# Kernel optimization log

Measured on AMD Instinct MI355X. Metric: run time of the kernel, lower is better.

The kernel has to match this reference:

```python
import jax, jax.numpy as jnp
import numpy as np

N = 20000      # total nodes (miRNA_number); first 504 are circRNAs
FM = 128       # feature dim (args.fm)
H = 8          # attention heads
OC = 128       # conv out_channels
E = 160000     # random edges (self loops added inside reference)
NEG_SLOPE = 0.2
CIRC = 504


def setup_inputs() -> dict:
    key = jax.random.key(0)
    ks = jax.random.split(key, 12)
    s_in = 1.0 / np.sqrt(FM)
    return {
        'x': jax.random.normal(ks[0], (N, FM), jnp.float32),
        'edge_index': jax.random.randint(ks[1], (2, E), 0, N, jnp.int64),
        'W1': jax.random.normal(ks[2], (FM, H * FM), jnp.float32) * s_in,
        'as1': jax.random.normal(ks[3], (H, FM), jnp.float32) * 0.1,
        'ad1': jax.random.normal(ks[4], (H, FM), jnp.float32) * 0.1,
        'b1': jnp.zeros((FM,), jnp.float32),
        'W2': jax.random.normal(ks[5], (FM, H * FM), jnp.float32) * s_in,
        'as2': jax.random.normal(ks[6], (H, FM), jnp.float32) * 0.1,
        'ad2': jax.random.normal(ks[7], (H, FM), jnp.float32) * 0.1,
        'b2': jnp.zeros((FM,), jnp.float32),
        'Wc': jax.random.normal(ks[8], (OC, 2, FM), jnp.float32) * s_in,
        'bc': jnp.zeros((OC,), jnp.float32),
    }


def gat_conv(x, src, dst, W, a_src, a_dst, b):
    # PyG GATConv, heads=H, concat=False (head mean), add_self_loops done by caller
    h = (x @ W).reshape(N, H, FM)                       # [N,H,F]
    s = jnp.einsum('nhf,hf->nh', h, a_src)              # alpha_src per node
    d = jnp.einsum('nhf,hf->nh', h, a_dst)              # alpha_dst per node
    e = jax.nn.leaky_relu(s[src] + d[dst], NEG_SLOPE)   # [E,H]
    m = jax.ops.segment_max(e, dst, num_segments=N)     # segment softmax (stable)
    ee = jnp.exp(e - m[dst])
    den = jax.ops.segment_sum(ee, dst, num_segments=N)
    alpha = ee / (den[dst] + 1e-16)                     # [E,H]
    out = jax.ops.segment_sum(h[src] * alpha[:, :, None], dst, num_segments=N)
    return out.mean(axis=1) + b                         # [N,F]


def reference(x, edge_index, W1, as1, ad1, b1, W2, as2, ad2, b2, Wc, bc):
    loops = jnp.arange(N, dtype=edge_index.dtype)
    src = jnp.concatenate([edge_index[0], loops])
    dst = jnp.concatenate([edge_index[1], loops])
    x1 = jax.nn.relu(gat_conv(x, src, dst, W1, as1, ad1, b1))
    x2 = jax.nn.relu(gat_conv(x1, src, dst, W2, as2, ad2, b2))
    # cat((x1,x2),dim=1).t().view(1, 2, FM, N) -> channels = [x1.T, x2.T]
    XM = jnp.stack([x1.T, x2.T], axis=0)                # [2,FM,N]
    feat = jnp.einsum('ckn,ock->on', XM, Wc) + bc[:, None]  # Conv1d kernel (FM,1)
    emb = feat.T                                        # [N,OC]
    circ, mir = emb[:CIRC], emb[CIRC:]
    return circ @ mir.T, circ, mir
```

## Files before the change

kernel.cpp:

```cpp
#include <hip/hip_runtime.h>
#include <math.h>

constexpr int NN   = 20000;
constexpr int FM   = 128;
constexpr int NH   = 8;
constexpr int HF   = NH * FM;
constexpr int EE   = 160000;
constexpr int ET   = EE + NN;
constexpr int OC   = 128;
constexpr int CIRC = 504;
constexpr int MIRN = NN - CIRC;
constexpr float NEG = 0.2f;

constexpr size_t OFF_CIRC = (size_t)CIRC * MIRN;
constexpr size_t OFF_MIR  = OFF_CIRC + (size_t)CIRC * OC;

typedef __attribute__((ext_vector_type(8))) short bf16x8;
typedef __attribute__((ext_vector_type(4))) float f32x4;

__device__ __forceinline__ int rl_i(int v, int lane) {
  return __builtin_amdgcn_readlane(v, lane);
}
__device__ __forceinline__ unsigned short bf16_rne(float x) {
  unsigned u = __float_as_uint(x);
  return (unsigned short)((u + 0x7FFFu + ((u >> 16) & 1u)) >> 16);
}
__device__ __forceinline__ float blo(unsigned u) { return __uint_as_float(u << 16); }
__device__ __forceinline__ float bhi(unsigned u) { return __uint_as_float(u & 0xFFFF0000u); }

__global__ void k_init_counts(int* __restrict__ cnt) {
  int i = blockIdx.x * blockDim.x + threadIdx.x;
  if (i < NN) cnt[i] = 1;
}

__global__ void k_count(const int* __restrict__ ei, int* __restrict__ cnt) {
  int e = blockIdx.x * blockDim.x + threadIdx.x;
  if (e < EE) atomicAdd(&cnt[ei[EE + e]], 1);
}

__global__ __launch_bounds__(1024) void k_scan(const int* __restrict__ cnt,
                                               int* __restrict__ rs,
                                               int* __restrict__ cur) {
  __shared__ int part[1024];
  const int t = threadIdx.x;
  const int SEG = (NN + 1023) / 1024;
  int lo = t * SEG, hi = min(NN, lo + SEG);
  int s = 0;
  for (int i = lo; i < hi; ++i) s += cnt[i];
  part[t] = s;
  __syncthreads();
  for (int off = 1; off < 1024; off <<= 1) {
    int v = 0;
    if (t >= off) v = part[t - off];
    __syncthreads();
    part[t] += v;
    __syncthreads();
  }
  int run = (t == 0) ? 0 : part[t - 1];
  for (int i = lo; i < hi; ++i) {
    int c = cnt[i];
    rs[i] = run;
    cur[i] = run;
    run += c;
  }
  if (t == 1023) rs[NN] = part[1023];
}

__global__ void k_fill(const int* __restrict__ ei, int* __restrict__ cur,
                       int* __restrict__ csrc) {
  int i = blockIdx.x * blockDim.x + threadIdx.x;
  if (i >= ET) return;
  int s, d;
  if (i < EE) { s = ei[i]; d = ei[EE + i]; }
  else        { s = i - EE; d = s; }
  int p = atomicAdd(&cur[d], 1);
  csrc[p] = s;
}

__global__ void k_prep_w(const float* __restrict__ W,
                         unsigned short* __restrict__ WThi,
                         unsigned short* __restrict__ WTlo) {
  int i = blockIdx.x * blockDim.x + threadIdx.x;
  if (i >= FM * HF) return;
  int k = i >> 10, n = i & 1023;
  float v = W[i];
  unsigned short h = bf16_rne(v);
  WThi[(size_t)n * FM + k] = h;
  WTlo[(size_t)n * FM + k] = bf16_rne(v - blo(h));
}

__global__ void k_split_x(const float* __restrict__ X,
                          unsigned short* __restrict__ Xhi,
                          unsigned short* __restrict__ Xlo) {
  int i = blockIdx.x * blockDim.x + threadIdx.x;
  if (i >= NN * FM) return;
  float v = X[i];
  unsigned short h = bf16_rne(v);
  Xhi[i] = h;
  Xlo[i] = bf16_rne(v - blo(h));
}

__global__ __launch_bounds__(256) void k_gemm_mfma(
    const unsigned short* __restrict__ Xhi, const unsigned short* __restrict__ Xlo,
    const unsigned short* __restrict__ WThi, const unsigned short* __restrict__ WTlo,
    const float* __restrict__ Asc, const float* __restrict__ Adc,
    unsigned short* __restrict__ H16, float* __restrict__ Sv,
    float* __restrict__ Dv) {
  const int lane = threadIdx.x & 63;
  const int wq   = threadIdx.x >> 6;
  const int m0   = blockIdx.x * 16;
  const int ri   = lane & 15;
  const int kg   = lane >> 4;

  bf16x8 Ah[4], Al[4];
  const unsigned short* xb = Xhi + (size_t)(m0 + ri) * FM + kg * 8;
  const unsigned short* xl = Xlo + (size_t)(m0 + ri) * FM + kg * 8;
#pragma unroll
  for (int ks = 0; ks < 4; ++ks) {
    Ah[ks] = *reinterpret_cast<const bf16x8*>(xb + ks * 32);
    Al[ks] = *reinterpret_cast<const bf16x8*>(xl + ks * 32);
  }
  float sacc[2][4] = {}, dacc[2][4] = {};
  for (int ct = 0; ct < 16; ++ct) {
    const int gc = wq * 256 + ct * 16 + ri;
    const unsigned short* wb = WThi + (size_t)gc * FM + kg * 8;
    const unsigned short* wl = WTlo + (size_t)gc * FM + kg * 8;
    f32x4 a0 = {0.f, 0.f, 0.f, 0.f}, a1 = a0, a2 = a0;
#pragma unroll
    for (int ks = 0; ks < 4; ++ks) {
      bf16x8 Bh = *reinterpret_cast<const bf16x8*>(wb + ks * 32);
      bf16x8 Bl = *reinterpret_cast<const bf16x8*>(wl + ks * 32);
      a0 = __builtin_amdgcn_mfma_f32_16x16x32_bf16(Ah[ks], Bh, a0, 0, 0, 0);
      a1 = __builtin_amdgcn_mfma_f32_16x16x32_bf16(Al[ks], Bh, a1, 0, 0, 0);
      a2 = __builtin_amdgcn_mfma_f32_16x16x32_bf16(Ah[ks], Bl, a2, 0, 0, 0);
    }
    const int hh = ct >> 3;
    const float as_ = Asc[(wq * 2 + hh) * FM + (gc & 127)];
    const float ad_ = Adc[(wq * 2 + hh) * FM + (gc & 127)];
#pragma unroll
    for (int r = 0; r < 4; ++r) {
      float v = a0[r] + a1[r] + a2[r];
      int m = m0 + kg * 4 + r;
      H16[(size_t)m * HF + gc] = bf16_rne(v);
      sacc[hh][r] += v * as_;
      dacc[hh][r] += v * ad_;
    }
  }
#pragma unroll
  for (int hh = 0; hh < 2; ++hh)
#pragma unroll
    for (int r = 0; r < 4; ++r) {
      float s = sacc[hh][r], d = dacc[hh][r];
#pragma unroll
      for (int mo = 1; mo <= 8; mo <<= 1) {
        s += __shfl_xor(s, mo, 64);
        d += __shfl_xor(d, mo, 64);
      }
      if (ri == 0) {
        int m = m0 + kg * 4 + r;
        Sv[m * NH + wq * 2 + hh] = s;
        Dv[m * NH + wq * 2 + hh] = d;
      }
    }
}

__global__ __launch_bounds__(256) void k_agg(const unsigned short* __restrict__ H16,
                                             const float* __restrict__ Sv,
                                             const float* __restrict__ Dv,
                                             const int* __restrict__ rs,
                                             const int* __restrict__ csrc,
                                             const float* __restrict__ bias,
                                             float* __restrict__ Xo,
                                             unsigned short* __restrict__ XhiO,
                                             unsigned short* __restrict__ XloO) {
  const int wave = threadIdx.x >> 6;
  const int lane = threadIdx.x & 63;
  const int n = blockIdx.x * 4 + wave;
  if (n >= NN) return;
  const int r0 = rs[n];
  const int deg = rs[n + 1] - r0;
  const int j = lane >> 3, h = lane & 7;
  const int h0 = lane >> 4;
  const int boff = h0 * FM + (lane & 15) * 8;
  const float dvh = Dv[n * 8 + h];

  float m = -INFINITY, l = 0.f;
  float4 acc[4];
#pragma unroll
  for (int q = 0; q < 4; ++q) acc[q] = make_float4(0.f, 0.f, 0.f, 0.f);

  for (int base = 0; base < deg; base += 8) {
    const int cnt = deg - base;
    int sj = csrc[r0 + min(base + j, deg - 1)];
    float lg = (j < cnt) ? (Sv[sj * 8 + h] + dvh) : -INFINITY;
    lg = lg > 0.f ? lg : NEG * lg;
    float cm = lg;
    cm = fmaxf(cm, __shfl_xor(cm, 8, 64));
    cm = fmaxf(cm, __shfl_xor(cm, 16, 64));
    cm = fmaxf(cm, __shfl_xor(cm, 32, 64));
    float mn = fmaxf(m, cm);
    float fs = expf(m - mn);
    float p = expf(lg - mn);
    float cs = p;
    cs += __shfl_xor(cs, 8, 64);
    cs += __shfl_xor(cs, 16, 64);
    cs += __shfl_xor(cs, 32, 64);
    l = l * fs + cs;
    m = mn;
    float f0 = __shfl(fs, h0, 64);
    float f1 = __shfl(fs, h0 + 4, 64);
    acc[0].x *= f0; acc[0].y *= f0; acc[0].z *= f0; acc[0].w *= f0;
    acc[1].x *= f0; acc[1].y *= f0; acc[1].z *= f0; acc[1].w *= f0;
    acc[2].x *= f1; acc[2].y *= f1; acc[2].z *= f1; acc[2].w *= f1;
    acc[3].x *= f1; acc[3].y *= f1; acc[3].z *= f1; acc[3].w *= f1;
#pragma unroll
    for (int jj = 0; jj < 8; ++jj) {
      if (jj < cnt) {
        int se = rl_i(sj, jj * 8);
        const uint4* hp = reinterpret_cast<const uint4*>(H16 + (size_t)se * HF + boff);
        uint4 v0 = hp[0];
        uint4 v1 = hp[64];
        float pe0 = __shfl(p, jj * 8 + h0, 64);
        float pe1 = __shfl(p, jj * 8 + h0 + 4, 64);
        acc[0].x += pe0 * blo(v0.x); acc[0].y += pe0 * bhi(v0.x);
        acc[0].z += pe0 * blo(v0.y); acc[0].w += pe0 * bhi(v0.y);
        acc[1].x += pe0 * blo(v0.z); acc[1].y += pe0 * bhi(v0.z);
        acc[1].z += pe0 * blo(v0.w); acc[1].w += pe0 * bhi(v0.w);
        acc[2].x += pe1 * blo(v1.x); acc[2].y += pe1 * bhi(v1.x);
        acc[2].z += pe1 * blo(v1.y); acc[2].w += pe1 * bhi(v1.y);
        acc[3].x += pe1 * blo(v1.z); acc[3].y += pe1 * bhi(v1.z);
        acc[3].z += pe1 * blo(v1.w); acc[3].w += pe1 * bhi(v1.w);
      }
    }
  }
  float inv0 = 1.0f / (__shfl(l, h0, 64) + 1e-16f);
  float inv1 = 1.0f / (__shfl(l, h0 + 4, 64) + 1e-16f);
  float o[8];
  o[0] = acc[0].x * inv0 + acc[2].x * inv1;
  o[1] = acc[0].y * inv0 + acc[2].y * inv1;
  o[2] = acc[0].z * inv0 + acc[2].z * inv1;
  o[3] = acc[0].w * inv0 + acc[2].w * inv1;
  o[4] = acc[1].x * inv0 + acc[3].x * inv1;
  o[5] = acc[1].y * inv0 + acc[3].y * inv1;
  o[6] = acc[1].z * inv0 + acc[3].z * inv1;
  o[7] = acc[1].w * inv0 + acc[3].w * inv1;
#pragma unroll
  for (int k = 0; k < 8; ++k) {
    o[k] += __shfl_xor(o[k], 16, 64);
    o[k] += __shfl_xor(o[k], 32, 64);
  }
  if (lane < 16) {
    const int f0i = lane * 8;
    float vals[8];
    union { unsigned short us[8]; uint4 v; } ph, pl;
#pragma unroll
    for (int k = 0; k < 8; ++k) {
      float bv = bias[f0i + k];
      vals[k] = fmaxf(o[k] * 0.125f + bv, 0.f);
      unsigned short hh = bf16_rne(vals[k]);
      ph.us[k] = hh;
      pl.us[k] = bf16_rne(vals[k] - blo(hh));
    }
    float4 w0 = make_float4(vals[0], vals[1], vals[2], vals[3]);
    float4 w1 = make_float4(vals[4], vals[5], vals[6], vals[7]);
    *reinterpret_cast<float4*>(Xo + (size_t)n * FM + f0i) = w0;
    *reinterpret_cast<float4*>(Xo + (size_t)n * FM + f0i + 4) = w1;
    *reinterpret_cast<uint4*>(XhiO + (size_t)n * FM + f0i) = ph.v;
    *reinterpret_cast<uint4*>(XloO + (size_t)n * FM + f0i) = pl.v;
  }
}

__global__ void k_transpose_wc(const float* __restrict__ Wc, float* __restrict__ WcT) {
  int i = blockIdx.x * blockDim.x + threadIdx.x;
  if (i < OC * 2 * FM) {
    int o = i / (2 * FM), k = i % (2 * FM);
    WcT[k * OC + o] = Wc[i];
  }
}

__global__ __launch_bounds__(256) void k_emb(const float* __restrict__ X1,
                                             const float* __restrict__ X2,
                                             const float* __restrict__ WcT,
                                             const float* __restrict__ bc,
                                             float* __restrict__ Out) {
  __shared__ float xs[64][129];
  const int t = threadIdx.x;
  const int row0 = blockIdx.x * 64;
  const int tr = (t >> 5) << 3;
  const int tc = (t & 31) << 2;
  float acc[8][4] = {};
  for (int half = 0; half < 2; ++half) {
    const float* Xs = half ? X2 : X1;
    __syncthreads();
#pragma unroll
    for (int it = 0; it < 8; ++it) {
      int f4 = it * 256 + t;
      int r = f4 >> 5;
      int c = (f4 & 31) << 2;
      int gr = row0 + r;
      float4 v = make_float4(0.f, 0.f, 0.f, 0.f);
      if (gr < NN) v = *reinterpret_cast<const float4*>(Xs + (size_t)gr * FM + c);
      xs[r][c] = v.x; xs[r][c + 1] = v.y; xs[r][c + 2] = v.z; xs[r][c + 3] = v.w;
    }
    __syncthreads();
    const float* Wp = WcT + (size_t)half * FM * OC;
    for (int kk = 0; kk < FM; ++kk) {
      float4 b = *reinterpret_cast<const float4*>(Wp + kk * OC + tc);
      float av[8];
#pragma unroll
      for (int r = 0; r < 8; ++r) av[r] = xs[tr + r][kk];
#pragma unroll
      for (int r = 0; r < 8; ++r) {
        acc[r][0] += av[r] * b.x;
        acc[r][1] += av[r] * b.y;
        acc[r][2] += av[r] * b.z;
        acc[r][3] += av[r] * b.w;
      }
    }
  }
  float4 bcv = *reinterpret_cast<const float4*>(bc + tc);
#pragma unroll
  for (int r = 0; r < 8; ++r) {
    int gr = row0 + tr + r;
    if (gr < NN) {
      float4 o;
      o.x = acc[r][0] + bcv.x;
      o.y = acc[r][1] + bcv.y;
      o.z = acc[r][2] + bcv.z;
      o.w = acc[r][3] + bcv.w;
      float* dst = (gr < CIRC)
                       ? (Out + OFF_CIRC + (size_t)gr * OC + tc)
                       : (Out + OFF_MIR + (size_t)(gr - CIRC) * OC + tc);
      *reinterpret_cast<float4*>(dst) = o;
    }
  }
}

__global__ __launch_bounds__(256) void k_outer(const float* __restrict__ A,
                                               const float* __restrict__ B,
                                               float* __restrict__ C) {
  __shared__ float As[64][65];
  __shared__ float Bs[64][65];
  const int t = threadIdx.x;
  const int i0 = blockIdx.y * 64;
  const int j0 = blockIdx.x * 64;
  const int tx = t & 15, ty = t >> 4;
  float acc[4][4] = {};
  for (int kh = 0; kh < 2; ++kh) {
    __syncthreads();
#pragma unroll
    for (int it = 0; it < 4; ++it) {
      int f4 = it * 256 + t;
      int r = f4 >> 4;
      int c = (f4 & 15) << 2;
      float4 v = make_float4(0.f, 0.f, 0.f, 0.f);
      if (i0 + r < CIRC)
        v = *reinterpret_cast<const float4*>(A + (size_t)(i0 + r) * OC + kh * 64 + c);
      As[r][c] = v.x; As[r][c + 1] = v.y; As[r][c + 2] = v.z; As[r][c + 3] = v.w;
      float4 w = make_float4(0.f, 0.f, 0.f, 0.f);
      if (j0 + r < MIRN)
        w = *reinterpret_cast<const float4*>(B + (size_t)(j0 + r) * OC + kh * 64 + c);
      Bs[r][c] = w.x; Bs[r][c + 1] = w.y; Bs[r][c + 2] = w.z; Bs[r][c + 3] = w.w;
    }
    __syncthreads();
    for (int kk = 0; kk < 64; ++kk) {
      float a[4], b[4];
#pragma unroll
      for (int r = 0; r < 4; ++r) a[r] = As[ty * 4 + r][kk];
#pragma unroll
      for (int c = 0; c < 4; ++c) b[c] = Bs[tx * 4 + c][kk];
#pragma unroll
      for (int r = 0; r < 4; ++r)
#pragma unroll
        for (int c = 0; c < 4; ++c) acc[r][c] += a[r] * b[c];
    }
  }
#pragma unroll
  for (int r = 0; r < 4; ++r) {
    int i = i0 + ty * 4 + r;
    if (i >= CIRC) break;
#pragma unroll
    for (int c = 0; c < 4; ++c) {
      int j = j0 + tx * 4 + c;
      if (j < MIRN) C[(size_t)i * MIRN + j] = acc[r][c];
    }
  }
}

static inline size_t alignup(size_t v) { return (v + 255) & ~(size_t)255; }

extern "C" void kernel_launch(void* const* d_in, const int* in_sizes, int n_in,
                              void* d_out, int out_size, void* d_ws, size_t ws_size,
                              hipStream_t stream) {
  const float* x   = (const float*)d_in[0];
  const int*   ei  = (const int*)d_in[1];
  const float* W1  = (const float*)d_in[2];
  const float* as1 = (const float*)d_in[3];
  const float* ad1 = (const float*)d_in[4];
  const float* b1  = (const float*)d_in[5];
  const float* W2  = (const float*)d_in[6];
  const float* as2 = (const float*)d_in[7];
  const float* ad2 = (const float*)d_in[8];
  const float* b2  = (const float*)d_in[9];
  const float* Wc  = (const float*)d_in[10];
  const float* bc  = (const float*)d_in[11];
  float* out = (float*)d_out;

  char* w = (char*)d_ws;
  size_t off = 0;
  unsigned short* H16  = (unsigned short*)(w + off); off = alignup(off + (size_t)NN * HF * 2);
  unsigned short* Xhi  = (unsigned short*)(w + off); off = alignup(off + (size_t)NN * FM * 2);
  unsigned short* Xlo  = (unsigned short*)(w + off); off = alignup(off + (size_t)NN * FM * 2);
  unsigned short* WThi = (unsigned short*)(w + off); off = alignup(off + (size_t)HF * FM * 2);
  unsigned short* WTlo = (unsigned short*)(w + off); off = alignup(off + (size_t)HF * FM * 2);
  float* Sbuf = (float*)(w + off); off = alignup(off + (size_t)NN * NH * 4);
  float* Dbuf = (float*)(w + off); off = alignup(off + (size_t)NN * NH * 4);
  float* X1   = (float*)(w + off); off = alignup(off + (size_t)NN * FM * 4);
  float* X2   = (float*)(w + off); off = alignup(off + (size_t)NN * FM * 4);
  float* WcT  = (float*)(w + off); off = alignup(off + (size_t)OC * 2 * FM * 4);
  int* counts = (int*)(w + off);   off = alignup(off + (size_t)NN * 4);
  int* rowst  = (int*)(w + off);   off = alignup(off + (size_t)(NN + 1) * 4);
  int* cursor = (int*)(w + off);   off = alignup(off + (size_t)NN * 4);
  int* csrsrc = (int*)(w + off);   off = alignup(off + (size_t)ET * 4);

  k_init_counts<<<(NN + 255) / 256, 256, 0, stream>>>(counts);
  k_count<<<(EE + 255) / 256, 256, 0, stream>>>(ei, counts);
  k_scan<<<1, 1024, 0, stream>>>(counts, rowst, cursor);
  k_fill<<<(ET + 255) / 256, 256, 0, stream>>>(ei, cursor, csrsrc);

  k_prep_w<<<(FM * HF + 255) / 256, 256, 0, stream>>>(W1, WThi, WTlo);
  k_split_x<<<(NN * FM + 255) / 256, 256, 0, stream>>>(x, Xhi, Xlo);
  k_gemm_mfma<<<NN / 16, 256, 0, stream>>>(Xhi, Xlo, WThi, WTlo, as1, ad1,
                                           H16, Sbuf, Dbuf);
  k_agg<<<(NN + 3) / 4, 256, 0, stream>>>(H16, Sbuf, Dbuf, rowst, csrsrc, b1,
                                          X1, Xhi, Xlo);
  k_prep_w<<<(FM * HF + 255) / 256, 256, 0, stream>>>(W2, WThi, WTlo);
  k_gemm_mfma<<<NN / 16, 256, 0, stream>>>(Xhi, Xlo, WThi, WTlo, as2, ad2,
                                           H16, Sbuf, Dbuf);
  k_agg<<<(NN + 3) / 4, 256, 0, stream>>>(H16, Sbuf, Dbuf, rowst, csrsrc, b2,
                                          X2, Xhi, Xlo);
  k_transpose_wc<<<(OC * 2 * FM + 255) / 256, 256, 0, stream>>>(Wc, WcT);
  k_emb<<<(NN + 63) / 64, 256, 0, stream>>>(X1, X2, WcT, bc, out);
  k_outer<<<dim3((MIRN + 63) / 64, (CIRC + 63) / 64), 256, 0, stream>>>(
      out + OFF_CIRC, out + OFF_MIR, out);
}
```

Measured before the change: 560.7 us.

## Retile projection GEMM into 64x64 per-wave tiles with atomic attention-score reduction

The feature-projection GEMM moves from 16-row blocks, where each wave streamed 256 columns, to a 2D grid in which each wave computes a 64x64 output tile from register-held A and B fragments. Each loaded fragment now feeds four MFMAs instead of one. Because a head's 128 columns are split across two waves, the per-node source and destination attention scores are accumulated with atomicAdd into buffers that a new kernel zeroes before each GEMM. This adds a zeroing launch and atomic traffic, raises register pressure from 16 accumulators, and makes the float summation order of the scores nondeterministic.

```diff
diff --git a/kernel.cpp b/kernel.cpp
--- a/kernel.cpp
+++ b/kernel.cpp
@@ -100,6 +100,11 @@
   Xlo[i] = bf16_rne(v - blo(h));
 }
 
+__global__ void k_zero_sd(float* __restrict__ Sv, float* __restrict__ Dv) {
+  int i = blockIdx.x * blockDim.x + threadIdx.x;
+  if (i < NN * NH) { Sv[i] = 0.f; Dv[i] = 0.f; }
+}
+
 __global__ __launch_bounds__(256) void k_gemm_mfma(
     const unsigned short* __restrict__ Xhi, const unsigned short* __restrict__ Xlo,
     const unsigned short* __restrict__ WThi, const unsigned short* __restrict__ WTlo,
@@ -107,61 +112,83 @@
     unsigned short* __restrict__ H16, float* __restrict__ Sv,
     float* __restrict__ Dv) {
   const int lane = threadIdx.x & 63;
-  const int wq   = threadIdx.x >> 6;
-  const int m0   = blockIdx.x * 16;
+  const int w    = threadIdx.x >> 6;
+  const int m0   = blockIdx.x * 64;
+  const int c0   = blockIdx.y * 256 + w * 64;
   const int ri   = lane & 15;
   const int kg   = lane >> 4;
 
-  bf16x8 Ah[4], Al[4];
-  const unsigned short* xb = Xhi + (size_t)(m0 + ri) * FM + kg * 8;
-  const unsigned short* xl = Xlo + (size_t)(m0 + ri) * FM + kg * 8;
-#pragma unroll
+  f32x4 acc[4][4];
+#pragma unroll
+  for (int mt = 0; mt < 4; ++mt)
+#pragma unroll
+    for (int nt = 0; nt < 4; ++nt) acc[mt][nt] = {0.f, 0.f, 0.f, 0.f};
+
   for (int ks = 0; ks < 4; ++ks) {
-    Ah[ks] = *reinterpret_cast<const bf16x8*>(xb + ks * 32);
-    Al[ks] = *reinterpret_cast<const bf16x8*>(xl + ks * 32);
-  }
-  float sacc[2][4] = {}, dacc[2][4] = {};
-  for (int ct = 0; ct < 16; ++ct) {
-    const int gc = wq * 256 + ct * 16 + ri;
-    const unsigned short* wb = WThi + (size_t)gc * FM + kg * 8;
-    const unsigned short* wl = WTlo + (size_t)gc * FM + kg * 8;
-    f32x4 a0 = {0.f, 0.f, 0.f, 0.f}, a1 = a0, a2 = a0;
-#pragma unroll
-    for (int ks = 0; ks < 4; ++ks) {
-      bf16x8 Bh = *reinterpret_cast<const bf16x8*>(wb + ks * 32);
-      bf16x8 Bl = *reinterpret_cast<const bf16x8*>(wl + ks * 32);
-      a0 = __builtin_amdgcn_mfma_f32_16x16x32_bf16(Ah[ks], Bh, a0, 0, 0, 0);
-      a1 = __builtin_amdgcn_mfma_f32_16x16x32_bf16(Al[ks], Bh, a1, 0, 0, 0);
-      a2 = __builtin_amdgcn_mfma_f32_16x16x32_bf16(Ah[ks], Bl, a2, 0, 0, 0);
-    }
-    const int hh = ct >> 3;
-    const float as_ = Asc[(wq * 2 + hh) * FM + (gc & 127)];
-    const float ad_ = Adc[(wq * 2 + hh) * FM + (gc & 127)];
+    const int ko = ks * 32 + kg * 8;
+    bf16x8 Ah[4], Al[4], Bh[4], Bl[4];
+#pragma unroll
+    for (int mt = 0; mt < 4; ++mt) {
+      int row = min(m0 + mt * 16 + ri, NN - 1);
+      Ah[mt] = *reinterpret_cast<const bf16x8*>(Xhi + (size_t)row * FM + ko);
+      Al[mt] = *reinterpret_cast<const bf16x8*>(Xlo + (size_t)row * FM + ko);
+    }
+#pragma unroll
+    for (int nt = 0; nt < 4; ++nt) {
+      int col = c0 + nt * 16 + ri;
+      Bh[nt] = *reinterpret_cast<const bf16x8*>(WThi + (size_t)col * FM + ko);
+      Bl[nt] = *reinterpret_cast<const bf16x8*>(WTlo + (size_t)col * FM + ko);
+    }
+#pragma unroll
+    for (int mt = 0; mt < 4; ++mt)
+#pragma unroll
+      for (int nt = 0; nt < 4; ++nt) {
+        acc[mt][nt] = __builtin_amdgcn_mfma_f32_16x16x32_bf16(Ah[mt], Bh[nt], acc[mt][nt], 0, 0, 0);
+        acc[mt][nt] = __builtin_amdgcn_mfma_f32_16x16x32_bf16(Al[mt], Bh[nt], acc[mt][nt], 0, 0, 0);
+        acc[mt][nt] = __builtin_amdgcn_mfma_f32_16x16x32_bf16(Ah[mt], Bl[nt], acc[mt][nt], 0, 0, 0);
+      }
+  }
+
+  const int hd   = c0 >> 7;
+  const int cih0 = c0 & 127;
+  float asv[4], adv[4];
+#pragma unroll
+  for (int nt = 0; nt < 4; ++nt) {
+    int cih = cih0 + nt * 16 + ri;
+    asv[nt] = Asc[hd * FM + cih];
+    adv[nt] = Adc[hd * FM + cih];
+  }
+#pragma unroll
+  for (int mt = 0; mt < 4; ++mt) {
+    float ssum[4] = {0.f, 0.f, 0.f, 0.f};
+    float dsum[4] = {0.f, 0.f, 0.f, 0.f};
+#pragma unroll
+    for (int nt = 0; nt < 4; ++nt) {
+      const int gc = c0 + nt * 16 + ri;
+#pragma unroll
+      for (int r = 0; r < 4; ++r) {
+        float v = acc[mt][nt][r];
+        int gr = m0 + mt * 16 + kg * 4 + r;
+        if (gr < NN) H16[(size_t)gr * HF + gc] = bf16_rne(v);
+        ssum[r] += v * asv[nt];
+        dsum[r] += v * adv[nt];
+      }
+    }
 #pragma unroll
     for (int r = 0; r < 4; ++r) {
-      float v = a0[r] + a1[r] + a2[r];
-      int m = m0 + kg * 4 + r;
-      H16[(size_t)m * HF + gc] = bf16_rne(v);
-      sacc[hh][r] += v * as_;
-      dacc[hh][r] += v * ad_;
-    }
-  }
-#pragma unroll
-  for (int hh = 0; hh < 2; ++hh)
-#pragma unroll
-    for (int r = 0; r < 4; ++r) {
-      float s = sacc[hh][r], d = dacc[hh][r];
+      float s = ssum[r], d = dsum[r];
 #pragma unroll
       for (int mo = 1; mo <= 8; mo <<= 1) {
         s += __shfl_xor(s, mo, 64);
         d += __shfl_xor(d, mo, 64);
       }
-      if (ri == 0) {
-        int m = m0 + kg * 4 + r;
-        Sv[m * NH + wq * 2 + hh] = s;
-        Dv[m * NH + wq * 2 + hh] = d;
-      }
-    }
+      int gr = m0 + mt * 16 + kg * 4 + r;
+      if (ri == 0 && gr < NN) {
+        atomicAdd(&Sv[gr * NH + hd], s);
+        atomicAdd(&Dv[gr * NH + hd], d);
+      }
+    }
+  }
 }
 
 __global__ __launch_bounds__(256) void k_agg(const unsigned short* __restrict__ H16,
@@ -428,15 +455,18 @@
   k_scan<<<1, 1024, 0, stream>>>(counts, rowst, cursor);
   k_fill<<<(ET + 255) / 256, 256, 0, stream>>>(ei, cursor, csrsrc);
 
+  dim3 gGemm((NN + 63) / 64, HF / 256);
   k_prep_w<<<(FM * HF + 255) / 256, 256, 0, stream>>>(W1, WThi, WTlo);
   k_split_x<<<(NN * FM + 255) / 256, 256, 0, stream>>>(x, Xhi, Xlo);
-  k_gemm_mfma<<<NN / 16, 256, 0, stream>>>(Xhi, Xlo, WThi, WTlo, as1, ad1,
-                                           H16, Sbuf, Dbuf);
+  k_zero_sd<<<(NN * NH + 255) / 256, 256, 0, stream>>>(Sbuf, Dbuf);
+  k_gemm_mfma<<<gGemm, 256, 0, stream>>>(Xhi, Xlo, WThi, WTlo, as1, ad1,
+                                         H16, Sbuf, Dbuf);
   k_agg<<<(NN + 3) / 4, 256, 0, stream>>>(H16, Sbuf, Dbuf, rowst, csrsrc, b1,
                                           X1, Xhi, Xlo);
   k_prep_w<<<(FM * HF + 255) / 256, 256, 0, stream>>>(W2, WThi, WTlo);
-  k_gemm_mfma<<<NN / 16, 256, 0, stream>>>(Xhi, Xlo, WThi, WTlo, as2, ad2,
-                                           H16, Sbuf, Dbuf);
+  k_zero_sd<<<(NN * NH + 255) / 256, 256, 0, stream>>>(Sbuf, Dbuf);
+  k_gemm_mfma<<<gGemm, 256, 0, stream>>>(Xhi, Xlo, WThi, WTlo, as2, ad2,
+                                         H16, Sbuf, Dbuf);
   k_agg<<<(NN + 3) / 4, 256, 0, stream>>>(H16, Sbuf, Dbuf, rowst, csrsrc, b2,
                                           X2, Xhi, Xlo);
   k_transpose_wc<<<(OC * 2 * FM + 255) / 256, 256, 0, stream>>>(Wc, WcT);
```

After: 516.1 us. 1.09x faster.
